# Kernel optimization log

Hardware: AMD Instinct MI355X
Metric: run time of the kernel (lower is better)

## Reference

```python
import jax, jax.numpy as jnp
import numpy as np

D_MODEL = 768
HEADS = 4
HEAD_DIM = D_MODEL // HEADS
SCALE = 20.0  # source divides scores by hard-coded 20
NEG = -1e9
LN_EPS = 1e-5


def setup_inputs() -> dict:
    key = jax.random.key(0)
    ks = jax.random.split(key, 8)
    B, S = 4, 2048
    x = jax.random.normal(ks[0], (B, S, D_MODEL), dtype=jnp.float32)
    attention_mask = jnp.zeros((B, 1, S), dtype=bool)  # no padding
    s = 1.0 / np.sqrt(D_MODEL)
    Wq = jax.random.normal(ks[1], (D_MODEL, D_MODEL), dtype=jnp.float32) * s
    Wk = jax.random.normal(ks[2], (D_MODEL, D_MODEL), dtype=jnp.float32) * s
    Wv = jax.random.normal(ks[3], (D_MODEL, D_MODEL), dtype=jnp.float32) * s
    bq = jnp.zeros((D_MODEL,), jnp.float32)
    bk = jnp.zeros((D_MODEL,), jnp.float32)
    bv = jnp.zeros((D_MODEL,), jnp.float32)
    gamma = jnp.ones((D_MODEL,), jnp.float32)
    beta = jnp.zeros((D_MODEL,), jnp.float32)
    return {"x": x, "attention_mask": attention_mask, "Wq": Wq, "bq": bq,
            "Wk": Wk, "bk": bk, "Wv": Wv, "bv": bv, "gamma": gamma, "beta": beta}


def _split_heads(t, B, S):
    return t.reshape(B, S, HEADS, HEAD_DIM).transpose(0, 2, 1, 3)  # [B,H,S,D]


def reference(x, attention_mask, Wq, bq, Wk, bk, Wv, bv, gamma, beta):
    B, S, _ = x.shape
    Q = _split_heads(x @ Wq.T + bq, B, S)
    K = _split_heads(x @ Wk.T + bk, B, S)
    V = _split_heads(x @ Wv.T + bv, B, S)
    # scores [B,H,Sq,Sk]
    w = jnp.einsum('bhqd,bhkd->bhqk', Q, K) / SCALE
    pad = attention_mask[:, :, :, None]                     # [B,1,S,1] -> broadcast
    look = jnp.triu(jnp.ones((S, S), dtype=bool), 1)        # strict upper triangle
    mask = look[None, None] | pad
    w = jnp.where(mask, NEG, w)
    # NOTE: source uses Softmax(dim=2), i.e. over the QUERY axis — kept faithfully
    attn = jax.nn.softmax(w, axis=2)
    x1 = jnp.einsum('bhqk,bhkd->bhqd', attn, V)             # [B,H,S,D]
    x1 = x1.transpose(0, 2, 1, 3).reshape(B, S, D_MODEL)
    y = x + x1
    mu = jnp.mean(y, axis=-1, keepdims=True)
    var = jnp.mean((y - mu) ** 2, axis=-1, keepdims=True)
    return (y - mu) * jax.lax.rsqrt(var + LN_EPS) * gamma + beta
```

## Files before the change

kernel.cpp:

```cpp
#include <hip/hip_runtime.h>

typedef _Float16 f16;
typedef _Float16 f16x8 __attribute__((ext_vector_type(8)));
typedef _Float16 f16x4 __attribute__((ext_vector_type(4)));
typedef float    f32x4 __attribute__((ext_vector_type(4)));

#define MFMA16(a,b,c) __builtin_amdgcn_mfma_f32_16x16x32_f16(a,b,c,0,0,0)

static constexpr float NEGV = -1e9f;
static constexpr float SC   = 0.05f;


__device__ __forceinline__ int poff(int qt){
    int m = qt>>1;
    return qt + m*(m-1) + ((qt&1) ? m : 0);
}

__device__ __forceinline__ void gload16(const void* g, void* l){
    __builtin_amdgcn_global_load_lds(
        (const __attribute__((address_space(1))) void*)g,
        (__attribute__((address_space(3))) void*)l, 16, 0, 0);
}

__global__ __launch_bounds__(256) void cvt_kernel(const float* __restrict__ in,
                                                  f16* __restrict__ out, int n){
    int i = (blockIdx.x*256 + threadIdx.x)*4;
    if (i < n){
        float4 v = *reinterpret_cast<const float4*>(in + i);
        f16x4 o = { (f16)v.x, (f16)v.y, (f16)v.z, (f16)v.w };
        *reinterpret_cast<f16x4*>(out + i) = o;
    }
}

__global__ __launch_bounds__(256) void cvtw_kernel(const float* __restrict__ a,
                                                   const float* __restrict__ b,
                                                   const float* __restrict__ c,
                                                   f16* __restrict__ out){
    int idx = blockIdx.x*256 + threadIdx.x;
    int which = idx / 147456;
    int r = idx - which*147456;
    const float* src = (which==0) ? a : (which==1 ? b : c);
    int i = r*4;
    float4 v = *reinterpret_cast<const float4*>(src + i);
    f16x4 o = { (f16)v.x, (f16)v.y, (f16)v.z, (f16)v.w };
    *reinterpret_cast<f16x4*>(out + (size_t)which*589824 + i) = o;
}

__global__ __launch_bounds__(256) void zero_kernel(float* __restrict__ p, int n){
    int i = (blockIdx.x*256 + threadIdx.x)*4;
    if (i < n){
        float4 z = {0.f,0.f,0.f,0.f};
        *reinterpret_cast<float4*>(p + i) = z;
    }
}

__global__ __launch_bounds__(256) void proj_kernel(
    const f16* __restrict__ xb, const f16* __restrict__ Wb,
    const float* __restrict__ bq, const float* __restrict__ bk, const float* __restrict__ bv,
    f16* __restrict__ Qb, f16* __restrict__ Kb, f16* __restrict__ Vt)
{
    __shared__ f16 As[2][128*32];
    __shared__ f16 Bs[2][128*32];
    const int z = blockIdx.z;
    const f16*   Wz   = Wb + (size_t)z*768*768;
    const float* bias = (z==0) ? bq : (z==1 ? bk : bv);
    f16*         out  = (z==0) ? Qb : (z==1 ? Kb : Vt);
    const int row0 = blockIdx.y*128, n0 = blockIdx.x*128;
    const int tid = threadIdx.x, w = tid>>6, l = tid&63;
    const int wm = w>>1, wn = w&1, c = l&15, g = l>>4;
    f32x4 zero = {0.f,0.f,0.f,0.f};
    f32x4 acc[4][4];
    for (int i=0;i<4;i++) for (int j=0;j<4;j++) acc[i][j] = zero;

    const f16* ag = xb + (size_t)(row0 + w*32 + (l>>2))*768 + (l&3)*8;
    const f16* bg = Wz + (size_t)(n0   + w*32 + (l>>2))*768 + (l&3)*8;

    auto stage = [&](int buf, int k0){
        gload16(ag + k0,          &As[buf][w*1024      ]);
        gload16(ag + k0 + 16*768, &As[buf][w*1024 + 512]);
        gload16(bg + k0,          &Bs[buf][w*1024      ]);
        gload16(bg + k0 + 16*768, &Bs[buf][w*1024 + 512]);
    };

    stage(0, 0);
    __syncthreads();
    for (int it=0; it<24; it++){
        int cur = it&1;
        if (it < 23) stage(cur^1, (it+1)*32);
        f16x8 af[4], bf[4];
        for (int mt=0; mt<4; mt++)
            af[mt] = *reinterpret_cast<const f16x8*>(&As[cur][(wm*64 + mt*16 + c)*32 + g*8]);
        for (int nt=0; nt<4; nt++)
            bf[nt] = *reinterpret_cast<const f16x8*>(&Bs[cur][(wn*64 + nt*16 + c)*32 + g*8]);
        for (int mt=0; mt<4; mt++)
            for (int nt=0; nt<4; nt++)
                acc[mt][nt] = MFMA16(af[mt], bf[nt], acc[mt][nt]);
        __syncthreads();
    }

    for (int nt=0; nt<4; nt++){
        int nb = n0 + wn*64 + nt*16;
        int h  = nb/192;
        int d  = (nb - h*192) + c;
        float bv_ = bias[nb + c];
        for (int mt=0; mt<4; mt++){
            int mb = row0 + wm*64 + mt*16 + g*4;
            int bi = mb>>11, s0 = mb&2047;
            int bh = bi*4 + h;
            if (z < 2){
                int ds = d>>5, gg = (d>>3)&3, e = d&7;
                for (int r=0;r<4;r++){
                    int s = s0 + r;
                    out[ ((size_t)(bh*128 + (s>>4))*6 + ds)*512 + ((gg*16) + (s&15))*8 + e ]
                        = (f16)(acc[mt][nt][r] + bv_);
                }
            } else {
                int dt = d>>4, cV = d&15;
                int kb64 = s0>>6, ks = (s0>>5)&1, gk = (s0>>3)&3, e0 = s0&7;
                f16x4 pk = { (f16)(acc[mt][nt][0] + bv_), (f16)(acc[mt][nt][1] + bv_),
                             (f16)(acc[mt][nt][2] + bv_), (f16)(acc[mt][nt][3] + bv_) };
                *reinterpret_cast<f16x4*>(
                    &out[ ((size_t)(bh*32 + kb64)*24 + dt*2 + ks)*512 + (gk*16 + cV)*8 + e0 ]) = pk;
            }
        }
    }
}

__global__ __launch_bounds__(512,4) void qkexp_kernel(
    const f16* __restrict__ Qb, const f16* __restrict__ Kb,
    const unsigned char* __restrict__ am,
    float* __restrict__ L, f16* __restrict__ Pg)
{
    __shared__ f16 Ks[2][24*512];
    __shared__ f16 Pl[8][16*32];
    const int bh = blockIdx.z, b = bh>>2;
    const int qb = blockIdx.x;
    const int ch = blockIdx.y;
    if (qb < 4*ch) return;
    const int tid = threadIdx.x, w = tid>>6, l = tid&63;
    const int c = l&15, g = l>>4;
    const int qt = qb*8 + w, qw = qt*16;
    const f16* Kfm = Kb + (size_t)bh*128*6*512;
    char* Pb = (char*)(&Pl[w][0]);
    f16* pw = Pg + ((size_t)bh*4160 + poff(qt))*512 + l*8;
    float* Lb = L + bh*2048;

    f16x8 qf[6];
    {
        const f16* qbase = Qb + ((size_t)(bh*128 + qt)*6)*512 + l*8;
        for (int ds=0; ds<6; ds++) qf[ds] = *reinterpret_cast<const f16x8*>(qbase + ds*512);
    }
    bool pm[4];
    for (int r=0;r<4;r++) pm[r] = am[b*2048 + qw + g*4 + r] != 0;

    f32x4 zero = {0.f,0.f,0.f,0.f};
    const int k00  = ch*512;
    const int kend = min(ch*512 + 512, qb*128 + 128);
    const int nt   = (kend - k00) >> 6;
    const int cid  = w*3;

    auto stage = [&](int buf, int k0){
        for (int i=0;i<3;i++){
            int ci = cid + i;
            int tl = ci/6, ds = ci - tl*6;
            gload16(Kfm + ((size_t)((k0>>4) + tl)*6 + ds)*512 + l*8, &Ks[buf][ci*512]);
        }
    };

    stage(0, k00);
    __syncthreads();
    for (int it=0; it<nt; it++){
        int cur = it&1;
        int k0  = k00 + it*64;
        if (it+1 < nt) stage(cur^1, k0 + 64);

        for (int half=0; half<2; half++){
            int kh = k0 + half*32;
            if (kh <= qw + 15){
                float cs[2];
                for (int kt2=0; kt2<2; kt2++){
                    int ktile = half*2 + kt2;
                    int kk = k0 + ktile*16;
                    f32x4 sacc = zero;
                    for (int ds=0; ds<6; ds++){
                        f16x8 kfr = *reinterpret_cast<const f16x8*>(&Ks[cur][(ktile*6+ds)*512 + l*8]);
                        sacc = MFMA16(qf[ds], kfr, sacc);
                    }
                    float csl = 0.f;
                    for (int r=0;r<4;r++){
                        int q = qw + g*4 + r;
                        float v = sacc[r]*SC;
                        if (pm[r]) v = NEGV;
                        float p = __expf(v);
                        if (kk + c > q) p = 0.f;
                        csl += p;
                        int row = g*4 + r;
                        int byo = (row*64 + (kt2*16 + c)*2) ^ ((row&3)<<4);
                        *reinterpret_cast<f16*>(Pb + byo) = (f16)p;
                    }
                    csl += __shfl_xor(csl, 16);
                    csl += __shfl_xor(csl, 32);
                    cs[kt2] = csl;
                }
                {
                    int byo = (c*64 + g*16) ^ ((c&3)<<4);
                    f16x8 pa = *reinterpret_cast<const f16x8*>(Pb + byo);
                    *reinterpret_cast<f16x8*>(pw + (size_t)(kh>>5)*512) = pa;
                }
                if (l < 32){
                    float csv = (l < 16) ? cs[0] : cs[1];
                    int kcol = kh + ((l < 16) ? 0 : 16) + (l & 15);
                    atomicAdd(&Lb[kcol], csv);
                }
            }
        }
        __syncthreads();
    }
}

__global__ __launch_bounds__(256) void scalev_kernel(f16* __restrict__ V, const float* __restrict__ L){
    int idx = blockIdx.x*256 + threadIdx.x;
    size_t base = (size_t)idx * 8;
    int bh = idx / 49152;
    int rem = idx - bh*49152;
    int chunk = rem >> 6;
    int sl = rem & 63;
    int kb64 = chunk/24, cr = chunk - kb64*24;
    int ks = cr & 1;
    int gk = sl >> 4;
    int k0 = kb64*64 + ks*32 + gk*8;
    const float* Lb = L + bh*2048 + k0;
    f16x8 v = *reinterpret_cast<f16x8*>(V + base);
    f16x8 o;
    for (int e=0;e<8;e++){
        float Lv = fmaxf(Lb[e], 1e-30f);
        o[e] = (f16)((float)v[e] / Lv);
    }
    *reinterpret_cast<f16x8*>(V + base) = o;
}

__global__ __launch_bounds__(512) void pv_kernel(
    const f16* __restrict__ Pg, const f16* __restrict__ Vt,
    float* __restrict__ x1)
{
    const int t  = blockIdx.x*8 + (threadIdx.x>>6);
    const int l  = threadIdx.x&63, c = l&15, g = l>>4;
    const int bh = t >> 8;
    const int r8 = t & 255;
    const int dh = r8 & 1;
    const int j  = r8 >> 1;
    const int qt = (j&1) ? (127 - (j>>1)) : (j>>1);
    const int b = bh>>2, h = bh&3;
    const int qw = qt*16;
    const f16* Vfm = Vt + (size_t)bh*32*24*512;
    const f16* pp  = Pg + ((size_t)bh*4160 + poff(qt))*512 + l*8;
    const int nc = (qt>>1) + 1;

    f32x4 zero = {0.f,0.f,0.f,0.f};
    f32x4 acc[6];
    for (int i=0;i<6;i++) acc[i] = zero;

    int kc = 0;
    for (; kc+1 < nc; kc += 2){
        const f16* pap = pp + (size_t)kc*512;
        f16x8 paA = *reinterpret_cast<const f16x8*>(pap);
        f16x8 paB = *reinterpret_cast<const f16x8*>(pap + 512);
        const f16* vb = Vfm + ((size_t)(kc>>1)*24 + dh*12)*512 + l*8;
        f16x8 vA[6], vB[6];
        #pragma unroll
        for (int d2=0; d2<6; d2++){
            vA[d2] = *reinterpret_cast<const f16x8*>(vb + d2*1024);
            vB[d2] = *reinterpret_cast<const f16x8*>(vb + d2*1024 + 512);
        }
        #pragma unroll
        for (int d2=0; d2<6; d2++) acc[d2] = MFMA16(paA, vA[d2], acc[d2]);
        #pragma unroll
        for (int d2=0; d2<6; d2++) acc[d2] = MFMA16(paB, vB[d2], acc[d2]);
    }
    if (kc < nc){
        f16x8 paA = *reinterpret_cast<const f16x8*>(pp + (size_t)kc*512);
        const f16* vb = Vfm + ((size_t)(kc>>1)*24 + dh*12)*512 + l*8;
        #pragma unroll
        for (int d2=0; d2<6; d2++){
            f16x8 vA = *reinterpret_cast<const f16x8*>(vb + d2*1024);
            acc[d2] = MFMA16(paA, vA, acc[d2]);
        }
    }

    for (int d2=0; d2<6; d2++){
        int d = h*192 + (dh*6 + d2)*16 + c;
        for (int r=0;r<4;r++){
            int q = qw + g*4 + r;
            x1[(size_t)(b*2048 + q)*768 + d] = acc[d2][r];
        }
    }
}

__global__ __launch_bounds__(256) void ln_kernel(
    const float* __restrict__ x, const float* __restrict__ x1,
    const float* __restrict__ gamma, const float* __restrict__ beta,
    float* __restrict__ out)
{
    const int r = blockIdx.x, t = threadIdx.x;
    const float* xr = x  + (size_t)r*768;
    const float* yr = x1 + (size_t)r*768;
    float v[3]; float s1 = 0.f, s2 = 0.f;
    for (int i=0;i<3;i++){ int j = t + i*256; float y = xr[j] + yr[j]; v[i]=y; s1+=y; s2+=y*y; }
    for (int o=32;o>=1;o>>=1){ s1 += __shfl_xor(s1,o); s2 += __shfl_xor(s2,o); }
    __shared__ float a1[4], a2[4];
    if ((t&63)==0){ a1[t>>6]=s1; a2[t>>6]=s2; }
    __syncthreads();
    s1 = a1[0]+a1[1]+a1[2]+a1[3];
    s2 = a2[0]+a2[1]+a2[2]+a2[3];
    float mu  = s1*(1.f/768.f);
    float var = s2*(1.f/768.f) - mu*mu;
    float rs  = rsqrtf(var + 1e-5f);
    for (int i=0;i<3;i++){
        int j = t + i*256;
        out[(size_t)r*768 + j] = (v[i]-mu)*rs*gamma[j] + beta[j];
    }
}

extern "C" void kernel_launch(void* const* d_in, const int* in_sizes, int n_in,
                              void* d_out, int out_size, void* d_ws, size_t ws_size,
                              hipStream_t stream)
{
    const float* x     = (const float*)d_in[0];
    const unsigned char* am = (const unsigned char*)d_in[1];
    const float* Wq    = (const float*)d_in[2];
    const float* bq    = (const float*)d_in[3];
    const float* Wk    = (const float*)d_in[4];
    const float* bk    = (const float*)d_in[5];
    const float* Wv    = (const float*)d_in[6];
    const float* bv    = (const float*)d_in[7];
    const float* gamma = (const float*)d_in[8];
    const float* beta  = (const float*)d_in[9];
    float* out = (float*)d_out;

    f16* xb  = (f16*)d_ws;
    f16* Wb  = xb + (size_t)8192*768;
    f16* Qb  = Wb + (size_t)3*768*768;
    f16* Kb  = Qb + (size_t)16*2048*192;
    f16* Vt  = Kb + (size_t)16*2048*192;
    f16* Pg  = Vt + (size_t)16*2048*192;
    float* L  = (float*)xb;
    float* x1 = (float*)Qb;

    cvt_kernel<<<6144, 256, 0, stream>>>(x,  xb, 8192*768);
    cvtw_kernel<<<1728, 256, 0, stream>>>(Wq, Wk, Wv, Wb);
    proj_kernel<<<dim3(6,64,3), 256, 0, stream>>>(xb, Wb, bq, bk, bv, Qb, Kb, Vt);
    zero_kernel<<<32, 256, 0, stream>>>(L, 16*2048);
    qkexp_kernel<<<dim3(16,4,16), 512, 0, stream>>>(Qb, Kb, am, L, Pg);
    scalev_kernel<<<3072, 256, 0, stream>>>(Vt, L);
    pv_kernel<<<512, 512, 0, stream>>>(Pg, Vt, x1);
    ln_kernel<<<8192, 256, 0, stream>>>(x, x1, gamma, beta, out);
}
```

Measured before the change: 282.4 us.

## Fuse conversions, fold V scaling into PV, remap proj blocks, stage Q/K stores

The x and weight fp32->fp16 conversions are merged into one launch, and the zero kernel is replaced with hipMemsetAsync. The separate scalev pass over V is removed: PV now scales each P fragment by the reciprocal column sum L as it loads it. The projection kernel remaps its block indices to spread neighbouring blocks across groups, and stages Q/K outputs in shared memory so they are written out as contiguous 16-byte stores. Together these cut launches and one full read-modify-write of V, but add per-fragment scaling ALU work and L loads inside the PV loop, and the approximate reciprocal may shift rounding slightly.

```diff
diff --git a/kernel.cpp b/kernel.cpp
--- a/kernel.cpp
+++ b/kernel.cpp
@@ -22,36 +22,26 @@
         (__attribute__((address_space(3))) void*)l, 16, 0, 0);
 }
 
-__global__ __launch_bounds__(256) void cvt_kernel(const float* __restrict__ in,
-                                                  f16* __restrict__ out, int n){
-    int i = (blockIdx.x*256 + threadIdx.x)*4;
-    if (i < n){
-        float4 v = *reinterpret_cast<const float4*>(in + i);
-        f16x4 o = { (f16)v.x, (f16)v.y, (f16)v.z, (f16)v.w };
-        *reinterpret_cast<f16x4*>(out + i) = o;
-    }
-}
-
-__global__ __launch_bounds__(256) void cvtw_kernel(const float* __restrict__ a,
-                                                   const float* __restrict__ b,
-                                                   const float* __restrict__ c,
-                                                   f16* __restrict__ out){
+__global__ __launch_bounds__(256) void cvtall_kernel(
+    const float* __restrict__ x,
+    const float* __restrict__ Wq, const float* __restrict__ Wk, const float* __restrict__ Wv,
+    f16* __restrict__ xb, f16* __restrict__ Wb)
+{
     int idx = blockIdx.x*256 + threadIdx.x;
-    int which = idx / 147456;
-    int r = idx - which*147456;
-    const float* src = (which==0) ? a : (which==1 ? b : c);
-    int i = r*4;
+    const float* src; f16* dst; int i;
+    if (idx < 1572864){
+        src = x; dst = xb; i = idx*4;
+    } else {
+        int widx = idx - 1572864;
+        int which = widx / 147456;
+        int r = widx - which*147456;
+        src = (which==0) ? Wq : (which==1 ? Wk : Wv);
+        dst = Wb + (size_t)which*589824;
+        i = r*4;
+    }
     float4 v = *reinterpret_cast<const float4*>(src + i);
     f16x4 o = { (f16)v.x, (f16)v.y, (f16)v.z, (f16)v.w };
-    *reinterpret_cast<f16x4*>(out + (size_t)which*589824 + i) = o;
-}
-
-__global__ __launch_bounds__(256) void zero_kernel(float* __restrict__ p, int n){
-    int i = (blockIdx.x*256 + threadIdx.x)*4;
-    if (i < n){
-        float4 z = {0.f,0.f,0.f,0.f};
-        *reinterpret_cast<float4*>(p + i) = z;
-    }
+    *reinterpret_cast<f16x4*>(dst + i) = o;
 }
 
 __global__ __launch_bounds__(256) void proj_kernel(
@@ -59,13 +49,18 @@
     const float* __restrict__ bq, const float* __restrict__ bk, const float* __restrict__ bv,
     f16* __restrict__ Qb, f16* __restrict__ Kb, f16* __restrict__ Vt)
 {
-    __shared__ f16 As[2][128*32];
-    __shared__ f16 Bs[2][128*32];
-    const int z = blockIdx.z;
+    __shared__ f16 shmem[16384];
+    const int lin = (blockIdx.z*64 + blockIdx.y)*6 + blockIdx.x;
+    const int idx = (lin & 7)*144 + (lin >> 3);
+    const int nx = idx % 6;
+    const int t2 = idx / 6;
+    const int ny = t2 & 63;
+    const int z  = t2 >> 6;
+
     const f16*   Wz   = Wb + (size_t)z*768*768;
     const float* bias = (z==0) ? bq : (z==1 ? bk : bv);
     f16*         out  = (z==0) ? Qb : (z==1 ? Kb : Vt);
-    const int row0 = blockIdx.y*128, n0 = blockIdx.x*128;
+    const int row0 = ny*128, n0 = nx*128;
     const int tid = threadIdx.x, w = tid>>6, l = tid&63;
     const int wm = w>>1, wn = w&1, c = l&15, g = l>>4;
     f32x4 zero = {0.f,0.f,0.f,0.f};
@@ -76,10 +71,12 @@
     const f16* bg = Wz + (size_t)(n0   + w*32 + (l>>2))*768 + (l&3)*8;
 
     auto stage = [&](int buf, int k0){
-        gload16(ag + k0,          &As[buf][w*1024      ]);
-        gload16(ag + k0 + 16*768, &As[buf][w*1024 + 512]);
-        gload16(bg + k0,          &Bs[buf][w*1024      ]);
-        gload16(bg + k0 + 16*768, &Bs[buf][w*1024 + 512]);
+        f16* As = shmem + buf*4096;
+        f16* Bs = shmem + 8192 + buf*4096;
+        gload16(ag + k0,          &As[w*1024      ]);
+        gload16(ag + k0 + 16*768, &As[w*1024 + 512]);
+        gload16(bg + k0,          &Bs[w*1024      ]);
+        gload16(bg + k0 + 16*768, &Bs[w*1024 + 512]);
     };
 
     stage(0, 0);
@@ -87,34 +84,53 @@
     for (int it=0; it<24; it++){
         int cur = it&1;
         if (it < 23) stage(cur^1, (it+1)*32);
+        const f16* As = shmem + cur*4096;
+        const f16* Bs = shmem + 8192 + cur*4096;
         f16x8 af[4], bf[4];
         for (int mt=0; mt<4; mt++)
-            af[mt] = *reinterpret_cast<const f16x8*>(&As[cur][(wm*64 + mt*16 + c)*32 + g*8]);
+            af[mt] = *reinterpret_cast<const f16x8*>(&As[(wm*64 + mt*16 + c)*32 + g*8]);
         for (int nt=0; nt<4; nt++)
-            bf[nt] = *reinterpret_cast<const f16x8*>(&Bs[cur][(wn*64 + nt*16 + c)*32 + g*8]);
+            bf[nt] = *reinterpret_cast<const f16x8*>(&Bs[(wn*64 + nt*16 + c)*32 + g*8]);
         for (int mt=0; mt<4; mt++)
             for (int nt=0; nt<4; nt++)
                 acc[mt][nt] = MFMA16(af[mt], bf[nt], acc[mt][nt]);
         __syncthreads();
     }
 
-    for (int nt=0; nt<4; nt++){
-        int nb = n0 + wn*64 + nt*16;
-        int h  = nb/192;
-        int d  = (nb - h*192) + c;
-        float bv_ = bias[nb + c];
-        for (int mt=0; mt<4; mt++){
-            int mb = row0 + wm*64 + mt*16 + g*4;
-            int bi = mb>>11, s0 = mb&2047;
-            int bh = bi*4 + h;
-            if (z < 2){
-                int ds = d>>5, gg = (d>>3)&3, e = d&7;
+    if (z < 2){
+        for (int nt=0; nt<4; nt++){
+            int nl = wn*64 + nt*16 + c;
+            float bv_ = bias[n0 + nl];
+            for (int mt=0; mt<4; mt++){
                 for (int r=0;r<4;r++){
-                    int s = s0 + r;
-                    out[ ((size_t)(bh*128 + (s>>4))*6 + ds)*512 + ((gg*16) + (s&15))*8 + e ]
-                        = (f16)(acc[mt][nt][r] + bv_);
+                    int ml = wm*64 + mt*16 + g*4 + r;
+                    int li = ((ml>>4)<<11) + ((nl>>5)<<9) + (((nl>>3)&3)<<7) + ((ml&15)<<3) + (nl&7);
+                    shmem[li] = (f16)(acc[mt][nt][r] + bv_);
                 }
-            } else {
+            }
+        }
+        __syncthreads();
+        const int bi = row0>>11, st0 = (row0&2047)>>4, bh0 = bi*4;
+        for (int cc=0; cc<8; cc++){
+            int chunk = cc*4 + w;
+            int tile = chunk>>2, seg = chunk&3;
+            f16x8 vv = *reinterpret_cast<const f16x8*>(&shmem[chunk*512 + l*8]);
+            int dglob = n0 + seg*32;
+            int h  = dglob/192;
+            int ds = (dglob - h*192)>>5;
+            *reinterpret_cast<f16x8*>(
+                out + ((size_t)((bh0 + h)*128 + st0 + tile)*6 + ds)*512 + l*8) = vv;
+        }
+    } else {
+        for (int nt=0; nt<4; nt++){
+            int nb = n0 + wn*64 + nt*16;
+            int h  = nb/192;
+            int d  = (nb - h*192) + c;
+            float bv_ = bias[nb + c];
+            for (int mt=0; mt<4; mt++){
+                int mb = row0 + wm*64 + mt*16 + g*4;
+                int bi = mb>>11, s0 = mb&2047;
+                int bh = bi*4 + h;
                 int dt = d>>4, cV = d&15;
                 int kb64 = s0>>6, ks = (s0>>5)&1, gk = (s0>>3)&3, e0 = s0&7;
                 f16x4 pk = { (f16)(acc[mt][nt][0] + bv_), (f16)(acc[mt][nt][1] + bv_),
@@ -218,30 +234,9 @@
     }
 }
 
-__global__ __launch_bounds__(256) void scalev_kernel(f16* __restrict__ V, const float* __restrict__ L){
-    int idx = blockIdx.x*256 + threadIdx.x;
-    size_t base = (size_t)idx * 8;
-    int bh = idx / 49152;
-    int rem = idx - bh*49152;
-    int chunk = rem >> 6;
-    int sl = rem & 63;
-    int kb64 = chunk/24, cr = chunk - kb64*24;
-    int ks = cr & 1;
-    int gk = sl >> 4;
-    int k0 = kb64*64 + ks*32 + gk*8;
-    const float* Lb = L + bh*2048 + k0;
-    f16x8 v = *reinterpret_cast<f16x8*>(V + base);
-    f16x8 o;
-    for (int e=0;e<8;e++){
-        float Lv = fmaxf(Lb[e], 1e-30f);
-        o[e] = (f16)((float)v[e] / Lv);
-    }
-    *reinterpret_cast<f16x8*>(V + base) = o;
-}
-
 __global__ __launch_bounds__(512) void pv_kernel(
     const f16* __restrict__ Pg, const f16* __restrict__ Vt,
-    float* __restrict__ x1)
+    const float* __restrict__ L, float* __restrict__ x1)
 {
     const int t  = blockIdx.x*8 + (threadIdx.x>>6);
     const int l  = threadIdx.x&63, c = l&15, g = l>>4;
@@ -254,7 +249,24 @@
     const int qw = qt*16;
     const f16* Vfm = Vt + (size_t)bh*32*24*512;
     const f16* pp  = Pg + ((size_t)bh*4160 + poff(qt))*512 + l*8;
+    const float* Lb = L + bh*2048 + g*8;
     const int nc = (qt>>1) + 1;
+
+    auto scale8 = [&](f16x8 p, int koff)->f16x8{
+        const float* Lp = Lb + koff;
+        f32x4 a  = *reinterpret_cast<const f32x4*>(Lp);
+        f32x4 b2 = *reinterpret_cast<const f32x4*>(Lp + 4);
+        f16x8 o;
+        o[0] = (f16)((float)p[0] * __builtin_amdgcn_rcpf(fmaxf(a[0],  1e-30f)));
+        o[1] = (f16)((float)p[1] * __builtin_amdgcn_rcpf(fmaxf(a[1],  1e-30f)));
+        o[2] = (f16)((float)p[2] * __builtin_amdgcn_rcpf(fmaxf(a[2],  1e-30f)));
+        o[3] = (f16)((float)p[3] * __builtin_amdgcn_rcpf(fmaxf(a[3],  1e-30f)));
+        o[4] = (f16)((float)p[4] * __builtin_amdgcn_rcpf(fmaxf(b2[0], 1e-30f)));
+        o[5] = (f16)((float)p[5] * __builtin_amdgcn_rcpf(fmaxf(b2[1], 1e-30f)));
+        o[6] = (f16)((float)p[6] * __builtin_amdgcn_rcpf(fmaxf(b2[2], 1e-30f)));
+        o[7] = (f16)((float)p[7] * __builtin_amdgcn_rcpf(fmaxf(b2[3], 1e-30f)));
+        return o;
+    };
 
     f32x4 zero = {0.f,0.f,0.f,0.f};
     f32x4 acc[6];
@@ -263,8 +275,8 @@
     int kc = 0;
     for (; kc+1 < nc; kc += 2){
         const f16* pap = pp + (size_t)kc*512;
-        f16x8 paA = *reinterpret_cast<const f16x8*>(pap);
-        f16x8 paB = *reinterpret_cast<const f16x8*>(pap + 512);
+        f16x8 paA = scale8(*reinterpret_cast<const f16x8*>(pap),       kc*32);
+        f16x8 paB = scale8(*reinterpret_cast<const f16x8*>(pap + 512), kc*32 + 32);
         const f16* vb = Vfm + ((size_t)(kc>>1)*24 + dh*12)*512 + l*8;
         f16x8 vA[6], vB[6];
         #pragma unroll
@@ -278,7 +290,7 @@
         for (int d2=0; d2<6; d2++) acc[d2] = MFMA16(paB, vB[d2], acc[d2]);
     }
     if (kc < nc){
-        f16x8 paA = *reinterpret_cast<const f16x8*>(pp + (size_t)kc*512);
+        f16x8 paA = scale8(*reinterpret_cast<const f16x8*>(pp + (size_t)kc*512), kc*32);
         const f16* vb = Vfm + ((size_t)(kc>>1)*24 + dh*12)*512 + l*8;
         #pragma unroll
         for (int d2=0; d2<6; d2++){
@@ -346,12 +358,10 @@
     float* L  = (float*)xb;
     float* x1 = (float*)Qb;
 
-    cvt_kernel<<<6144, 256, 0, stream>>>(x,  xb, 8192*768);
-    cvtw_kernel<<<1728, 256, 0, stream>>>(Wq, Wk, Wv, Wb);
+    cvtall_kernel<<<7872, 256, 0, stream>>>(x, Wq, Wk, Wv, xb, Wb);
     proj_kernel<<<dim3(6,64,3), 256, 0, stream>>>(xb, Wb, bq, bk, bv, Qb, Kb, Vt);
-    zero_kernel<<<32, 256, 0, stream>>>(L, 16*2048);
+    hipMemsetAsync(L, 0, 16*2048*sizeof(float), stream);
     qkexp_kernel<<<dim3(16,4,16), 512, 0, stream>>>(Qb, Kb, am, L, Pg);
-    scalev_kernel<<<3072, 256, 0, stream>>>(Vt, L);
-    pv_kernel<<<512, 512, 0, stream>>>(Pg, Vt, x1);
+    pv_kernel<<<512, 512, 0, stream>>>(Pg, Vt, L, x1);
     ln_kernel<<<8192, 256, 0, stream>>>(x, x1, gamma, beta, out);
 }
```

Result: faster. 271.4 us (-3.9%).
